# Kernel optimization log

Hardware: AMD Instinct MI355X
Metric: run time of the kernel (lower is better)

## Reference

```python
import jax, jax.numpy as jnp
import numpy as np

NUM_USERS = 100000
NUM_ITEMS = 50000
DIM = 64
HOP = 3
NNZ = 4_000_000
BATCH = 4096
NUM_NEG = 8
N = NUM_USERS + NUM_ITEMS


def setup_inputs() -> dict:
    key = jax.random.key(0)
    ks = jax.random.split(key, 8)
    user_emb = jax.random.normal(ks[0], (NUM_USERS, DIM), dtype=jnp.float32) * 0.1
    item_emb = jax.random.normal(ks[1], (NUM_ITEMS, DIM), dtype=jnp.float32) * 0.1
    # normalized-Laplacian-like small positive values
    A_vals = jax.random.uniform(ks[2], (NNZ,), dtype=jnp.float32) * 0.02
    A_rows = jax.random.randint(ks[3], (NNZ,), 0, N, dtype=jnp.int32)
    A_cols = jax.random.randint(ks[4], (NNZ,), 0, N, dtype=jnp.int32)
    users = jax.random.randint(ks[5], (BATCH,), 0, NUM_USERS, dtype=jnp.int32)
    items = jax.random.randint(ks[6], (BATCH,), 0, NUM_ITEMS, dtype=jnp.int32)
    negatives = jax.random.randint(ks[7], (NUM_NEG * BATCH,), 0, NUM_ITEMS, dtype=jnp.int32)
    return {"user_emb": user_emb, "item_emb": item_emb, "A_vals": A_vals,
            "A_rows": A_rows, "A_cols": A_cols,
            "users": users, "items": items, "negatives": negatives}


def _computer(user_emb, item_emb, A_vals, A_rows, A_cols):
    # LightGCN propagation: x_{k+1} = A @ x_k, mean over hops 0..HOP
    all_emb = jnp.concatenate([user_emb, item_emb], axis=0)  # [N, D]
    x = all_emb
    acc = all_emb
    for _ in range(HOP):
        # SpMM: gather source rows, scale by edge value, scatter-add to dest
        msgs = A_vals[:, None] * x[A_cols]                      # [nnz, D]
        x = jax.ops.segment_sum(msgs, A_rows, num_segments=N)   # [N, D]
        acc = acc + x
    light_out = acc / jnp.asarray(HOP + 1, dtype=all_emb.dtype)
    return light_out[:NUM_USERS], light_out[NUM_USERS:]


def reference(user_emb, item_emb, A_vals, A_rows, A_cols, users, items, negatives):
    all_users_emb, all_items_emb = _computer(user_emb, item_emb, A_vals, A_rows, A_cols)
    users_emb = all_users_emb[users]          # [B, D]
    items_emb = all_items_emb[items]          # [B, D]
    neg_item_embs = all_items_emb[negatives]  # [NUM_NEG*B, D]
    pos_scores = jnp.sum(users_emb * items_emb, axis=1)  # [B]
    pos_exp = jnp.exp(pos_scores)
    neg_k = jnp.sum(users_emb[None, :, :] * neg_item_embs.reshape(NUM_NEG, BATCH, DIM), axis=-1)  # [NUM_NEG, B]
    neg_exp = jnp.sum(jnp.exp(neg_k), axis=0)  # [B]
    info_nce = jnp.mean(-jnp.log(pos_exp / (pos_exp + neg_exp)))
    return info_nce
```

## Files before the change

### kernel.cpp

```cpp
#include <hip/hip_runtime.h>
#include <hip/hip_bf16.h>
#include <hip/hip_fp8.h>


#define NUM_USERS 100000
#define NUM_ITEMS 50000
#define NTOT      150000
#define DIM       64
#define NNZ_C     4000000
#define BATCH     4096
#define NUM_NEG   8
#define NSLICE    (BATCH + BATCH + NUM_NEG * BATCH)

#define RPB        768
#define NBUCKET    ((NTOT + RPB - 1) / RPB)
#define CAP        25600
#define CAPC       24832
#define BIN_BLOCKS 1024
#define EPB        ((NNZ_C + BIN_BLOCKS - 1) / BIN_BLOCKS)
#define NLOSSB     (BATCH * 64 / 256)

using fp8t = __hip_fp8_e4m3;

typedef unsigned int u32x4 __attribute__((ext_vector_type(4)));
typedef float        f32x2 __attribute__((ext_vector_type(2)));

__device__ __forceinline__ float f8dec(unsigned char b) {
    fp8t h; h.__x = (__hip_fp8_storage_t)b; return (float)h;
}
__device__ __forceinline__ unsigned char f8enc(float f) {
    fp8t h(f); return (unsigned char)h.__x;
}

__device__ __forceinline__ void fp8x4_fma(unsigned int q, float w, float* a) {
#if __has_builtin(__builtin_amdgcn_cvt_pk_f32_fp8)
    f32x2 lo = __builtin_amdgcn_cvt_pk_f32_fp8((int)q, false);
    f32x2 hi = __builtin_amdgcn_cvt_pk_f32_fp8((int)q, true);
    a[0] = fmaf(w, lo.x, a[0]);
    a[1] = fmaf(w, lo.y, a[1]);
    a[2] = fmaf(w, hi.x, a[2]);
    a[3] = fmaf(w, hi.y, a[3]);
#else
    a[0] = fmaf(w, f8dec((unsigned char)(q       & 0xFF)), a[0]);
    a[1] = fmaf(w, f8dec((unsigned char)((q>>8)  & 0xFF)), a[1]);
    a[2] = fmaf(w, f8dec((unsigned char)((q>>16) & 0xFF)), a[2]);
    a[3] = fmaf(w, f8dec((unsigned char)((q>>24) & 0xFF)), a[3]);
#endif
}

__global__ void convert_concat(const float* __restrict__ ue, const float* __restrict__ ie,
                               unsigned char* __restrict__ x0, int* __restrict__ bcur) {
    int i = blockIdx.x * blockDim.x + threadIdx.x;
    if (i < NBUCKET) bcur[i * 16] = i * CAP;
    if (i >= NTOT * DIM / 4) return;
    float4 v = (i * 4 < NUM_USERS * DIM)
                   ? ((const float4*)ue)[i]
                   : ((const float4*)ie)[i - NUM_USERS * DIM / 4];
    uchar4 o;
    o.x = f8enc(v.x); o.y = f8enc(v.y); o.z = f8enc(v.z); o.w = f8enc(v.w);
    ((uchar4*)x0)[i] = o;
}

__global__ void __launch_bounds__(256) bin_k(const int* __restrict__ rows,
                                             const int* __restrict__ cols,
                                             const float* __restrict__ vals,
                                             int* __restrict__ bcur,
                                             int2* __restrict__ brec) {
    __shared__ int2 stage[EPB];
    __shared__ int  lh[NBUCKET], gbase[NBUCKET];
    __shared__ unsigned short lofs[NBUCKET];
    int t = threadIdx.x;
    int* sm = (int*)stage;
    int e0 = blockIdx.x * EPB;
    int e1 = e0 + EPB; if (e1 > NNZ_C) e1 = NNZ_C;
    for (int i = t; i < NBUCKET; i += 256) lh[i] = 0;
    __syncthreads();
    #pragma unroll 4
    for (int e = e0 + t; e < e1; e += 256)
        atomicAdd(&lh[rows[e] / RPB], 1);
    __syncthreads();
    {
        int ssum = (t < NBUCKET) ? lh[t] : 0;
        sm[t] = ssum;
        __syncthreads();
        for (int o = 1; o < 256; o <<= 1) {
            int v = (t >= o) ? sm[t - o] : 0;
            __syncthreads();
            sm[t] += v;
            __syncthreads();
        }
        if (t < NBUCKET) lofs[t] = (unsigned short)(sm[t] - ssum);
    }
    __syncthreads();
    for (int i = t; i < NBUCKET; i += 256) {
        int c = lh[i];
        if (c) {
            int c8 = (c + 7) & ~7;
            gbase[i] = atomicAdd(&bcur[i * 16], c8);
        }
        lh[i] = 0;
    }
    __syncthreads();
    #pragma unroll 2
    for (int e = e0 + t; e < e1; e += 256) {
        int   r = rows[e];
        int   c = __builtin_nontemporal_load(cols + e);
        float v = __builtin_nontemporal_load(vals + e);
        int b = r / RPB;
        int rank = atomicAdd(&lh[b], 1);
        int j = (int)lofs[b] + rank;
        unsigned int v14 = (unsigned int)lrintf(v * 524288.0f);
        if (v14 > 16383u) v14 = 16383u;
        stage[j] = make_int2((int)((v14 << 18) | (unsigned int)c), r);
    }
    __syncthreads();
    int cnt = e1 - e0;
    for (int j = t; j < cnt; j += 256) {
        int2 rc = stage[j];
        int b = rc.y / RPB;
        brec[gbase[b] + (j - (int)lofs[b])] = rc;
    }
    for (int i = t; i < NBUCKET; i += 256) {
        int c = lh[i];
        if (c) {
            int c8 = (c + 7) & ~7;
            int g  = gbase[i];
            for (int q = g + c; q < g + c8; ++q)
                brec[q] = make_int2(0, -1);
        }
    }
}

__global__ void __launch_bounds__(512) csr_fix_k(const int2* __restrict__ brec,
                                                 const int* __restrict__ bcur,
                                                 unsigned int* __restrict__ crec,
                                                 int2* __restrict__ rp2) {
    __shared__ int lh[RPB], lb[RPB], lc[RPB], sm2[512];
    int b = blockIdx.x;
    int t = threadIdx.x;
    int s = b * CAP, e = bcur[b * 16];
    int cnt = e - s;
    int cb = b * CAPC;
    int rbase = b * RPB;
    for (int i = t; i < RPB; i += 512) lh[i] = 0;
    __syncthreads();
    for (int j = t; j < cnt; j += 512) {
        unsigned int rl = (unsigned int)(brec[s + j].y - rbase);
        if (rl < RPB) atomicAdd(&lh[rl], 1);
    }
    __syncthreads();
    {
        int loc[2];
        int ssum = 0;
        #pragma unroll
        for (int k = 0; k < 2; ++k) {
            int i = t * 2 + k;
            loc[k] = (i < RPB) ? ((lh[i] + 7) & ~7) : 0;
            ssum += loc[k];
        }
        sm2[t] = ssum;
        __syncthreads();
        for (int o = 1; o < 512; o <<= 1) {
            int v = (t >= o) ? sm2[t - o] : 0;
            __syncthreads();
            sm2[t] += v;
            __syncthreads();
        }
        int run = sm2[t] - ssum;
        #pragma unroll
        for (int k = 0; k < 2; ++k) {
            int i = t * 2 + k;
            if (i < RPB) {
                lb[i] = run;
                lc[i] = 0;
                int row = rbase + i;
                if (row < NTOT) rp2[row] = make_int2(cb + run, cb + run + lh[i]);
            }
            run += loc[k];
        }
    }
    __syncthreads();
    for (int j = t; j < cnt; j += 512) {
        int2 rc = brec[s + j];
        unsigned int rl = (unsigned int)(rc.y - rbase);
        if (rl < RPB) {
            int pos = atomicAdd(&lc[rl], 1);
            crec[cb + lb[rl] + pos] = (unsigned int)rc.x;
        }
    }
    __syncthreads();
    for (int i = t; i < RPB; i += 512) {
        int base = cb + lb[i];
        int c8 = (lh[i] + 7) & ~7;
        for (int q = lh[i]; q < c8; ++q) crec[base + q] = 0u;
    }
}

__device__ __forceinline__ void spmm_row_v4(const unsigned char* __restrict__ x,
                                            const unsigned int* __restrict__ crec,
                                            int s, int e, int lane, float* acc) {
    const float c19 = 1.9073486328125e-6f;
    int g  = lane >> 4;
    int dq = (lane & 15) * 4;
    acc[0] = acc[1] = acc[2] = acc[3] = 0.0f;
    int e8 = s + ((e - s + 7) & ~7);
    for (int j = s + 8 * g; j < e8; j += 32) {
        u32x4 pa = __builtin_nontemporal_load((const u32x4*)(crec + j));
        u32x4 pb = __builtin_nontemporal_load((const u32x4*)(crec + j + 4));
        unsigned int q0 = *(const unsigned int*)(x + (pa.x & 0x3FFFFu) * DIM + dq);
        unsigned int q1 = *(const unsigned int*)(x + (pa.y & 0x3FFFFu) * DIM + dq);
        unsigned int q2 = *(const unsigned int*)(x + (pa.z & 0x3FFFFu) * DIM + dq);
        unsigned int q3 = *(const unsigned int*)(x + (pa.w & 0x3FFFFu) * DIM + dq);
        unsigned int q4 = *(const unsigned int*)(x + (pb.x & 0x3FFFFu) * DIM + dq);
        unsigned int q5 = *(const unsigned int*)(x + (pb.y & 0x3FFFFu) * DIM + dq);
        unsigned int q6 = *(const unsigned int*)(x + (pb.z & 0x3FFFFu) * DIM + dq);
        unsigned int q7 = *(const unsigned int*)(x + (pb.w & 0x3FFFFu) * DIM + dq);
        float w0 = (float)(pa.x >> 18) * c19;
        float w1 = (float)(pa.y >> 18) * c19;
        float w2 = (float)(pa.z >> 18) * c19;
        float w3 = (float)(pa.w >> 18) * c19;
        float w4 = (float)(pb.x >> 18) * c19;
        float w5 = (float)(pb.y >> 18) * c19;
        float w6 = (float)(pb.z >> 18) * c19;
        float w7 = (float)(pb.w >> 18) * c19;
        fp8x4_fma(q0, w0, acc);
        fp8x4_fma(q1, w1, acc);
        fp8x4_fma(q2, w2, acc);
        fp8x4_fma(q3, w3, acc);
        fp8x4_fma(q4, w4, acc);
        fp8x4_fma(q5, w5, acc);
        fp8x4_fma(q6, w6, acc);
        fp8x4_fma(q7, w7, acc);
    }
    acc[0] += __shfl_xor(acc[0], 16, 64);
    acc[1] += __shfl_xor(acc[1], 16, 64);
    acc[2] += __shfl_xor(acc[2], 16, 64);
    acc[3] += __shfl_xor(acc[3], 16, 64);
    acc[0] += __shfl_xor(acc[0], 32, 64);
    acc[1] += __shfl_xor(acc[1], 32, 64);
    acc[2] += __shfl_xor(acc[2], 32, 64);
    acc[3] += __shfl_xor(acc[3], 32, 64);
}

__device__ __forceinline__ void spmm_store(unsigned char* __restrict__ y, int row,
                                           int lane, const float* acc) {
    if (lane < 16) {
        uchar4 o;
        o.x = f8enc(acc[0] * 16.0f);
        o.y = f8enc(acc[1] * 16.0f);
        o.z = f8enc(acc[2] * 16.0f);
        o.w = f8enc(acc[3] * 16.0f);
        *(uchar4*)(y + row * DIM + lane * 4) = o;
    }
}

__global__ void spmm_k(const unsigned char* __restrict__ x, const int2* __restrict__ rp2,
                       const unsigned int* __restrict__ crec, unsigned char* __restrict__ y) {
    int row  = (blockIdx.x * blockDim.x + threadIdx.x) >> 6;
    int lane = threadIdx.x & 63;
    if (row >= NTOT) return;
    int2 se = rp2[row];
    float acc[4];
    spmm_row_v4(x, crec, se.x, se.y, lane, acc);
    spmm_store(y, row, lane, acc);
}

__global__ void spmm_sliced_k(const unsigned char* __restrict__ x, const int2* __restrict__ rp2,
                              const unsigned int* __restrict__ crec,
                              const int* __restrict__ users, const int* __restrict__ items,
                              const int* __restrict__ negs, unsigned char* __restrict__ y) {
    int w    = (blockIdx.x * blockDim.x + threadIdx.x) >> 6;
    int lane = threadIdx.x & 63;
    if (w >= NSLICE) return;
    int row = (w < BATCH)     ? users[w]
            : (w < 2 * BATCH) ? NUM_USERS + items[w - BATCH]
                              : NUM_USERS + negs[w - 2 * BATCH];
    int2 se = rp2[row];
    float acc[4];
    spmm_row_v4(x, crec, se.x, se.y, lane, acc);
    spmm_store(y, row, lane, acc);
}

__global__ void loss_k(const unsigned char* __restrict__ x0, const unsigned char* __restrict__ x1,
                       const unsigned char* __restrict__ x2, const unsigned char* __restrict__ x3,
                       const int* __restrict__ users, const int* __restrict__ items,
                       const int* __restrict__ negs, float* __restrict__ partials) {
    __shared__ float psum[4];
    int w    = (blockIdx.x * blockDim.x + threadIdx.x) >> 6;
    int lane = threadIdx.x & 63;
    int wv   = threadIdx.x >> 6;
    float v = 0.0f;
    if (w < BATCH) {
        auto rowv = [&](int r) -> float {
            int o = r * DIM + lane;
            return 0.25f * f8dec(x0[o]) + 0.015625f * f8dec(x1[o]) +
                   9.765625e-4f * f8dec(x2[o]) + 6.103515625e-5f * f8dec(x3[o]);
        };
        float ue = rowv(users[w]);
        float ie = rowv(NUM_USERS + items[w]);
        float p = ue * ie;
        for (int o = 32; o > 0; o >>= 1) p += __shfl_xor(p, o, 64);
        float pe = expf(p);
        float ne = 0.0f;
        for (int k = 0; k < NUM_NEG; ++k) {
            float q = ue * rowv(NUM_USERS + negs[k * BATCH + w]);
            for (int o = 32; o > 0; o >>= 1) q += __shfl_xor(q, o, 64);
            ne += expf(q);
        }
        v = logf((pe + ne) / pe);
    }
    if (lane == 0) psum[wv] = v;
    __syncthreads();
    if (threadIdx.x == 0)
        partials[blockIdx.x] = psum[0] + psum[1] + psum[2] + psum[3];
}

__global__ void finalize_k(const float* __restrict__ partials, float* __restrict__ out) {
    __shared__ float ps[4];
    int t = threadIdx.x;
    float s = 0.0f;
    for (int i = t; i < NLOSSB; i += 256) s += partials[i];
    for (int o = 32; o > 0; o >>= 1) s += __shfl_xor(s, o, 64);
    if ((t & 63) == 0) ps[t >> 6] = s;
    __syncthreads();
    if (t == 0) out[0] = (ps[0] + ps[1] + ps[2] + ps[3]) * (1.0f / BATCH);
}

__global__ void sentinel_k(float* __restrict__ out) {
    out[0] = -1.0f;
}

extern "C" void kernel_launch(void* const* d_in, const int* in_sizes, int n_in,
                              void* d_out, int out_size, void* d_ws, size_t ws_size,
                              hipStream_t stream) {
    const float* user_emb = (const float*)d_in[0];
    const float* item_emb = (const float*)d_in[1];
    const float* A_vals   = (const float*)d_in[2];
    const int*   A_rows   = (const int*)d_in[3];
    const int*   A_cols   = (const int*)d_in[4];
    const int*   users    = (const int*)d_in[5];
    const int*   items    = (const int*)d_in[6];
    const int*   negs     = (const int*)d_in[7];
    float* out = (float*)d_out;

    char* ws = (char*)d_ws;
    size_t off = 0;
    auto carve = [&](size_t bytes) -> char* {
        char* p = ws + off;
        off = (off + bytes + 255) & ~(size_t)255;
        return p;
    };
    unsigned char* x0 = (unsigned char*)carve((size_t)NTOT * DIM);
    unsigned char* x1 = (unsigned char*)carve((size_t)NTOT * DIM);
    unsigned char* x2 = (unsigned char*)carve((size_t)NTOT * DIM);
    unsigned char* x3 = (unsigned char*)carve((size_t)NTOT * DIM);
    int2*  brec       = (int2*)carve((size_t)NBUCKET * CAP * 8);
    unsigned int* crec= (unsigned int*)carve((size_t)NBUCKET * CAPC * 4 + 1024);
    int2*  rp2        = (int2*)carve((size_t)NTOT * 8);
    int*   bcur       = (int*)carve((size_t)NBUCKET * 64);
    float* partials   = (float*)carve((size_t)NLOSSB * 4);

    if (off > ws_size) {
        sentinel_k<<<1, 1, 0, stream>>>(out);
        return;
    }

    convert_concat<<<(NTOT * DIM / 4 + 255) / 256, 256, 0, stream>>>(user_emb, item_emb, x0, bcur);

    bin_k<<<BIN_BLOCKS, 256, 0, stream>>>(A_rows, A_cols, A_vals, bcur, brec);
    csr_fix_k<<<NBUCKET, 512, 0, stream>>>(brec, bcur, crec, rp2);

    const int spmm_blocks = (NTOT * 64 + 255) / 256;
    spmm_k<<<spmm_blocks, 256, 0, stream>>>(x0, rp2, crec, x1);
    spmm_k<<<spmm_blocks, 256, 0, stream>>>(x1, rp2, crec, x2);
    spmm_sliced_k<<<(NSLICE * 64 + 255) / 256, 256, 0, stream>>>(x2, rp2, crec, users, items, negs, x3);

    loss_k<<<NLOSSB, 256, 0, stream>>>(x0, x1, x2, x3, users, items, negs, partials);
    finalize_k<<<1, 256, 0, stream>>>(partials, out);
}
```

Before: 359.6 us.

## Fuse final reduction into loss kernel and fold weight scale into store

The final-reduction kernel is removed. The last loss block to finish, detected with an atomic counter that convert_concat resets, now sums the per-block partials. The SpMM inner loop drops the per-edge multiply by the weight dequantization constant and applies one combined scale when the row is stored. The binning kernel packs the bucket index into the high bits of the row field, which replaces an integer division with a shift in the scatter loop. The trade-offs are an extra atomic and fence per loss block, and a changed point where the fp8 scaling is applied.

Result: slower. 377.6 us (+5.0%).

```diff
diff --git a/kernel.cpp b/kernel.cpp
--- a/kernel.cpp
+++ b/kernel.cpp
@@ -19,6 +19,7 @@
 #define BIN_BLOCKS 1024
 #define EPB        ((NNZ_C + BIN_BLOCKS - 1) / BIN_BLOCKS)
 #define NLOSSB     (BATCH * 64 / 256)
+#define SCALE_ST   3.0517578125e-5f
 
 using fp8t = __hip_fp8_e4m3;
 
@@ -49,8 +50,10 @@
 }
 
 __global__ void convert_concat(const float* __restrict__ ue, const float* __restrict__ ie,
-                               unsigned char* __restrict__ x0, int* __restrict__ bcur) {
+                               unsigned char* __restrict__ x0, int* __restrict__ bcur,
+                               int* __restrict__ done) {
     int i = blockIdx.x * blockDim.x + threadIdx.x;
+    if (i == 0) done[0] = 0;
     if (i < NBUCKET) bcur[i * 16] = i * CAP;
     if (i >= NTOT * DIM / 4) return;
     float4 v = (i * 4 < NUM_USERS * DIM)
@@ -111,13 +114,14 @@
         int j = (int)lofs[b] + rank;
         unsigned int v14 = (unsigned int)lrintf(v * 524288.0f);
         if (v14 > 16383u) v14 = 16383u;
-        stage[j] = make_int2((int)((v14 << 18) | (unsigned int)c), r);
+        stage[j] = make_int2((int)((v14 << 18) | (unsigned int)c),
+                             (b << 18) | r);
     }
     __syncthreads();
     int cnt = e1 - e0;
     for (int j = t; j < cnt; j += 256) {
         int2 rc = stage[j];
-        int b = rc.y / RPB;
+        int b = (int)((unsigned int)rc.y >> 18);
         brec[gbase[b] + (j - (int)lofs[b])] = rc;
     }
     for (int i = t; i < NBUCKET; i += 256) {
@@ -145,7 +149,7 @@
     for (int i = t; i < RPB; i += 512) lh[i] = 0;
     __syncthreads();
     for (int j = t; j < cnt; j += 512) {
-        unsigned int rl = (unsigned int)(brec[s + j].y - rbase);
+        unsigned int rl = (unsigned int)((brec[s + j].y & 0x3FFFF) - rbase);
         if (rl < RPB) atomicAdd(&lh[rl], 1);
     }
     __syncthreads();
@@ -182,7 +186,7 @@
     __syncthreads();
     for (int j = t; j < cnt; j += 512) {
         int2 rc = brec[s + j];
-        unsigned int rl = (unsigned int)(rc.y - rbase);
+        unsigned int rl = (unsigned int)((rc.y & 0x3FFFF) - rbase);
         if (rl < RPB) {
             int pos = atomicAdd(&lc[rl], 1);
             crec[cb + lb[rl] + pos] = (unsigned int)rc.x;
@@ -199,7 +203,6 @@
 __device__ __forceinline__ void spmm_row_v4(const unsigned char* __restrict__ x,
                                             const unsigned int* __restrict__ crec,
                                             int s, int e, int lane, float* acc) {
-    const float c19 = 1.9073486328125e-6f;
     int g  = lane >> 4;
     int dq = (lane & 15) * 4;
     acc[0] = acc[1] = acc[2] = acc[3] = 0.0f;
@@ -215,14 +218,14 @@
         unsigned int q5 = *(const unsigned int*)(x + (pb.y & 0x3FFFFu) * DIM + dq);
         unsigned int q6 = *(const unsigned int*)(x + (pb.z & 0x3FFFFu) * DIM + dq);
         unsigned int q7 = *(const unsigned int*)(x + (pb.w & 0x3FFFFu) * DIM + dq);
-        float w0 = (float)(pa.x >> 18) * c19;
-        float w1 = (float)(pa.y >> 18) * c19;
-        float w2 = (float)(pa.z >> 18) * c19;
-        float w3 = (float)(pa.w >> 18) * c19;
-        float w4 = (float)(pb.x >> 18) * c19;
-        float w5 = (float)(pb.y >> 18) * c19;
-        float w6 = (float)(pb.z >> 18) * c19;
-        float w7 = (float)(pb.w >> 18) * c19;
+        float w0 = (float)(pa.x >> 18);
+        float w1 = (float)(pa.y >> 18);
+        float w2 = (float)(pa.z >> 18);
+        float w3 = (float)(pa.w >> 18);
+        float w4 = (float)(pb.x >> 18);
+        float w5 = (float)(pb.y >> 18);
+        float w6 = (float)(pb.z >> 18);
+        float w7 = (float)(pb.w >> 18);
         fp8x4_fma(q0, w0, acc);
         fp8x4_fma(q1, w1, acc);
         fp8x4_fma(q2, w2, acc);
@@ -246,10 +249,10 @@
                                            int lane, const float* acc) {
     if (lane < 16) {
         uchar4 o;
-        o.x = f8enc(acc[0] * 16.0f);
-        o.y = f8enc(acc[1] * 16.0f);
-        o.z = f8enc(acc[2] * 16.0f);
-        o.w = f8enc(acc[3] * 16.0f);
+        o.x = f8enc(acc[0] * SCALE_ST);
+        o.y = f8enc(acc[1] * SCALE_ST);
+        o.z = f8enc(acc[2] * SCALE_ST);
+        o.w = f8enc(acc[3] * SCALE_ST);
         *(uchar4*)(y + row * DIM + lane * 4) = o;
     }
 }
@@ -284,8 +287,10 @@
 __global__ void loss_k(const unsigned char* __restrict__ x0, const unsigned char* __restrict__ x1,
                        const unsigned char* __restrict__ x2, const unsigned char* __restrict__ x3,
                        const int* __restrict__ users, const int* __restrict__ items,
-                       const int* __restrict__ negs, float* __restrict__ partials) {
+                       const int* __restrict__ negs, float* __restrict__ partials,
+                       int* __restrict__ done, float* __restrict__ out) {
     __shared__ float psum[4];
+    __shared__ float ps2[4];
     int w    = (blockIdx.x * blockDim.x + threadIdx.x) >> 6;
     int lane = threadIdx.x & 63;
     int wv   = threadIdx.x >> 6;
@@ -311,19 +316,27 @@
     }
     if (lane == 0) psum[wv] = v;
     __syncthreads();
-    if (threadIdx.x == 0)
-        partials[blockIdx.x] = psum[0] + psum[1] + psum[2] + psum[3];
-}
-
-__global__ void finalize_k(const float* __restrict__ partials, float* __restrict__ out) {
-    __shared__ float ps[4];
-    int t = threadIdx.x;
-    float s = 0.0f;
-    for (int i = t; i < NLOSSB; i += 256) s += partials[i];
-    for (int o = 32; o > 0; o >>= 1) s += __shfl_xor(s, o, 64);
-    if ((t & 63) == 0) ps[t >> 6] = s;
-    __syncthreads();
-    if (t == 0) out[0] = (ps[0] + ps[1] + ps[2] + ps[3]) * (1.0f / BATCH);
+    if (threadIdx.x == 0) {
+        float bp = psum[0] + psum[1] + psum[2] + psum[3];
+        __hip_atomic_store(&partials[blockIdx.x], bp, __ATOMIC_RELAXED,
+                           __HIP_MEMORY_SCOPE_AGENT);
+        __threadfence();
+        int old = atomicAdd(done, 1);
+        psum[0] = (old == NLOSSB - 1) ? 1.0f : 0.0f;
+    }
+    __syncthreads();
+    if (psum[0] != 0.0f) {
+        __threadfence();
+        int t = threadIdx.x;
+        float s = 0.0f;
+        for (int i = t; i < NLOSSB; i += 256)
+            s += __hip_atomic_load(&partials[i], __ATOMIC_RELAXED,
+                                   __HIP_MEMORY_SCOPE_AGENT);
+        for (int o = 32; o > 0; o >>= 1) s += __shfl_xor(s, o, 64);
+        if ((t & 63) == 0) ps2[t >> 6] = s;
+        __syncthreads();
+        if (t == 0) out[0] = (ps2[0] + ps2[1] + ps2[2] + ps2[3]) * (1.0f / BATCH);
+    }
 }
 
 __global__ void sentinel_k(float* __restrict__ out) {
@@ -359,13 +372,14 @@
     int2*  rp2        = (int2*)carve((size_t)NTOT * 8);
     int*   bcur       = (int*)carve((size_t)NBUCKET * 64);
     float* partials   = (float*)carve((size_t)NLOSSB * 4);
+    int*   done       = (int*)carve(256);
 
     if (off > ws_size) {
         sentinel_k<<<1, 1, 0, stream>>>(out);
         return;
     }
 
-    convert_concat<<<(NTOT * DIM / 4 + 255) / 256, 256, 0, stream>>>(user_emb, item_emb, x0, bcur);
+    convert_concat<<<(NTOT * DIM / 4 + 255) / 256, 256, 0, stream>>>(user_emb, item_emb, x0, bcur, done);
 
     bin_k<<<BIN_BLOCKS, 256, 0, stream>>>(A_rows, A_cols, A_vals, bcur, brec);
     csr_fix_k<<<NBUCKET, 512, 0, stream>>>(brec, bcur, crec, rp2);
@@ -375,6 +389,5 @@
     spmm_k<<<spmm_blocks, 256, 0, stream>>>(x1, rp2, crec, x2);
     spmm_sliced_k<<<(NSLICE * 64 + 255) / 256, 256, 0, stream>>>(x2, rp2, crec, users, items, negs, x3);
 
-    loss_k<<<NLOSSB, 256, 0, stream>>>(x0, x1, x2, x3, users, items, negs, partials);
-    finalize_k<<<1, 256, 0, stream>>>(partials, out);
-}
+    loss_k<<<NLOSSB, 256, 0, stream>>>(x0, x1, x2, x3, users, items, negs, partials, done, out);
+}
```
